# Optimization experiments

Hardware: AMD Instinct MI355X
Metric: run time of the kernel (lower is better)

Reference implementation:

```python
import jax, jax.numpy as jnp
import numpy as np
import math

L = 7          # spherical-harmonic truncation -> lsize = (L+1)^2 = 64
T = 128        # number of channels/fragments in clms


def _cg_coef(j1, m1, j2, m2, j, m):
    """Clebsch-Gordan coefficient <j1 m1 j2 m2 | j m> via the Racah formula."""
    if m1 + m2 != m or not (abs(j1 - j2) <= j <= j1 + j2):
        return 0.0
    f = math.factorial
    pref = math.sqrt((2 * j + 1) * f(j1 + j2 - j) * f(j1 - j2 + j)
                     * f(-j1 + j2 + j) / f(j1 + j2 + j + 1))
    pref *= math.sqrt(f(j + m) * f(j - m) * f(j1 - m1) * f(j1 + m1)
                      * f(j2 - m2) * f(j2 + m2))
    kmin = max(0, j2 - j - m1, j1 + m2 - j)
    kmax = min(j1 + j2 - j, j1 - m1, j2 + m2)
    s = 0.0
    for k in range(kmin, kmax + 1):
        s += (-1) ** k / (f(k) * f(j1 + j2 - j - k) * f(j1 - m1 - k)
                          * f(j2 + m2 - k) * f(j - j2 + m1 + k) * f(j - j1 - m2 + k))
    return pref * s


def _idx(l, m):
    return l * l + l + m


def _build_C(L):
    """Dense packed CG tensor C[(l,m),(l1,m1),(l2,m2)], zero outside selection rules."""
    lsize = (L + 1) ** 2
    C = np.zeros((lsize, lsize, lsize), dtype=np.float64)
    for l1 in range(L + 1):
        for l2 in range(L + 1):
            for l in range(abs(l1 - l2), min(l1 + l2, L) + 1):
                for m1 in range(-l1, l1 + 1):
                    for m2 in range(-l2, l2 + 1):
                        m = m1 + m2
                        if abs(m) <= l:
                            C[_idx(l, m), _idx(l1, m1), _idx(l2, m2)] = \
                                _cg_coef(l1, m1, l2, m2, l, m)
    return C.astype(np.float32)


def setup_inputs() -> dict:
    key = jax.random.key(0)
    clms = jax.random.normal(key, ((L + 1) ** 2, T), dtype=jnp.float32)
    C = jnp.asarray(_build_C(L))
    return {"clms": clms, "C": C}


def reference(clms, C):
    lsize = clms.shape[0]
    Lc = int(math.isqrt(lsize)) - 1
    Tn = clms.shape[1]
    # full Kronecker product, blockwise indexed by (l1,m1),(l2,m2); [lsize, lsize, T^2]
    Gs = (clms[:, None, :, None] * clms[None, :, None, :]).reshape(lsize, lsize, Tn * Tn)
    temp = [[] for _ in range(Lc + 1)]
    for l1 in range(Lc + 1):
        for l2 in range(Lc + 1):
            g = Gs[l1 * l1:(l1 + 1) ** 2, l2 * l2:(l2 + 1) ** 2, :]
            cg = C[:, l1 * l1:(l1 + 1) ** 2, l2 * l2:(l2 + 1) ** 2]
            # cg @ g over the flattened (m1,m2) block -> [(Lc+1)^2, T^2]
            prod = jnp.einsum('kij,ijt->kt', cg, g)
            for l in range(abs(l1 - l2), min(l1 + l2, Lc) + 1):
                temp[l].append(prod[l * l:(l + 1) ** 2, :])
    return tuple(jnp.concatenate(t, axis=1) for t in temp)
```

## Files before the change

### kernel.cpp

```cpp
#include <hip/hip_runtime.h>

#define TDIM 128

__device__ __forceinline__ float u2f(unsigned int u) {
  union { unsigned int u; float f; } w; w.u = u; return w.f;
}
__device__ __forceinline__ float bf2f(unsigned short v) {
  return u2f(((unsigned int)v) << 16);
}
__device__ __forceinline__ unsigned short f2bf(float x) {
  union { float f; unsigned int u; } w; w.f = x;
  unsigned int u = w.u;
  u += 0x7fffu + ((u >> 16) & 1u);
  return (unsigned short)(u >> 16);
}

__global__ __launch_bounds__(256, 4)
void cg_kernel(const void* __restrict__ clms_raw,
               const void* __restrict__ C_raw,
               void* __restrict__ out_raw) {
  __shared__ float sa[16 * TDIM];
  __shared__ float sb[16 * TDIM];

  const int tid = threadIdx.x;

  const unsigned int* cw = (const unsigned int*)clms_raw;
  int nbf = 0;
  #pragma unroll
  for (int i = 0; i < 32; ++i) {
    unsigned int e = (cw[i] >> 7) & 0xFFu;
    nbf += (e >= 110u && e <= 135u) ? 1 : 0;
  }
  const bool in_bf16 = (nbf >= 16);
  const bool c_bf16 = ((*(const unsigned int*)C_raw) & 0xffffu) == 0x3f80u;

  const int r = blockIdx.x;
  int l = 0, cum = 0, pc = 8;
  if (r >= 8)    { l = 1; cum = 8;    pc = 21; }
  if (r >= 71)   { l = 2; cum = 71;   pc = 31; }
  if (r >= 226)  { l = 3; cum = 226;  pc = 38; }
  if (r >= 492)  { l = 4; cum = 492;  pc = 42; }
  if (r >= 870)  { l = 5; cum = 870;  pc = 43; }
  if (r >= 1343) { l = 6; cum = 1343; pc = 41; }
  if (r >= 1876) { l = 7; cum = 1876; pc = 36; }
  const int rem = r - cum;
  const int mi  = rem / pc;
  const int m   = mi - l;
  int pp = rem - mi * pc;
  int l1 = 0, l2 = 0, found = 0;
  #pragma unroll
  for (int a = 0; a < 8; ++a) {
    int d = a - l; if (d < 0) d = -d;
    int hi = a + l; if (hi > 7) hi = 7;
    int na = hi - d + 1;
    if (!found && pp < na) { l1 = a; l2 = d + pp; found = 1; }
    if (!found) pp -= na;
  }

  const int m1lo = (-l1 > m - l2) ? -l1 : (m - l2);
  const int m1hi = ( l1 < m + l2) ?  l1 : (m + l2);
  const int nnz = m1hi - m1lo + 1;
  const int i0 = l1 * (l1 + 1) + m1lo;
  const int j0 = l2 * (l2 + 1) + (m - m1lo);
  const int k0 = l * (l + 1) + m;

  #pragma unroll
  for (int kk = 0; kk < 8; ++kk) {
    const int u = tid + 256 * kk;
    if (u < 1920) {
      const int row  = u >> 6;
      const int lane = u & 63;
      const int isB  = row >= 15;
      const int q    = isB ? row - 15 : row;
      const int qc   = (q < nnz) ? q : 0;
      const int gr   = isB ? (j0 - qc) : (i0 + qc);
      float f0, f1;
      if (in_bf16) {
        unsigned int v = ((const unsigned int*)clms_raw)[gr * 64 + lane];
        f0 = u2f(v << 16); f1 = u2f(v & 0xffff0000u);
      } else {
        float2 v = ((const float2*)clms_raw)[gr * 64 + lane];
        f0 = v.x; f1 = v.y;
      }
      if (isB) {
        float cq = 0.0f;
        if (q < nnz) {
          int ci = (k0 * 64 + i0 + q) * 64 + (j0 - q);
          cq = c_bf16 ? bf2f(((const unsigned short*)C_raw)[ci])
                      : ((const float*)C_raw)[ci];
        }
        f0 *= cq; f1 *= cq;
        *(float2*)&sb[q * TDIM + lane * 2] = make_float2(f0, f1);
      } else {
        *(float2*)&sa[q * TDIM + lane * 2] = make_float2(f0, f1);
      }
    }
  }
  __syncthreads();

  const int tx = tid & 31;
  const int ty = tid >> 5;
  float4 b[15];
  #pragma unroll
  for (int q = 0; q < 15; ++q)
    b[q] = *(const float4*)&sb[q * TDIM + tx * 4];

  const unsigned long long outbase =
      (unsigned long long)r * (TDIM * TDIM) + (unsigned int)(tx * 4);

  if (in_bf16) {
    unsigned short* out = (unsigned short*)out_raw;
    for (int s0 = 0; s0 < 4; ++s0) {
      const int t1b = ty + 32 * s0;
      float4 acc[4];
      #pragma unroll
      for (int d = 0; d < 4; ++d) acc[d] = make_float4(0.f, 0.f, 0.f, 0.f);
      #pragma unroll
      for (int q = 0; q < 15; ++q) {
        if (q < nnz) {
          #pragma unroll
          for (int d = 0; d < 4; ++d) {
            float a = sa[q * TDIM + t1b + 8 * d];
            acc[d].x += a * b[q].x;
            acc[d].y += a * b[q].y;
            acc[d].z += a * b[q].z;
            acc[d].w += a * b[q].w;
          }
        }
      }
      #pragma unroll
      for (int d = 0; d < 4; ++d) {
        ushort4 o;
        o.x = f2bf(acc[d].x); o.y = f2bf(acc[d].y);
        o.z = f2bf(acc[d].z); o.w = f2bf(acc[d].w);
        *(ushort4*)(out + outbase + (unsigned long long)((t1b + 8 * d) * TDIM)) = o;
      }
    }
  } else {
    float* out = (float*)out_raw;
    for (int s0 = 0; s0 < 4; ++s0) {
      const int t1b = ty + 32 * s0;
      float4 acc[4];
      #pragma unroll
      for (int d = 0; d < 4; ++d) acc[d] = make_float4(0.f, 0.f, 0.f, 0.f);
      #pragma unroll
      for (int q = 0; q < 15; ++q) {
        if (q < nnz) {
          #pragma unroll
          for (int d = 0; d < 4; ++d) {
            float a = sa[q * TDIM + t1b + 8 * d];
            acc[d].x += a * b[q].x;
            acc[d].y += a * b[q].y;
            acc[d].z += a * b[q].z;
            acc[d].w += a * b[q].w;
          }
        }
      }
      #pragma unroll
      for (int d = 0; d < 4; ++d)
        *(float4*)(out + outbase + (unsigned long long)((t1b + 8 * d) * TDIM)) = acc[d];
    }
  }
}

extern "C" void kernel_launch(void* const* d_in, const int* in_sizes, int n_in,
                              void* d_out, int out_size, void* d_ws, size_t ws_size,
                              hipStream_t stream) {
  (void)in_sizes; (void)n_in; (void)d_ws; (void)ws_size;
  const int nrows = out_size / (TDIM * TDIM);
  cg_kernel<<<nrows, 256, 0, stream>>>(d_in[0], d_in[1], d_out);
}
```

Measured before the change: 165.9 us.

## Use persistent blocks that stage all of clms in shared memory once

Launches at most 1024 blocks that each copy the full clms matrix into shared memory once, then grid-stride over output rows. The per-row global gather of A and B rows and the associated barrier are replaced by direct shared-memory indexing, with CG coefficients applied when forming the B registers. This trades a larger shared-memory footprint per block, and so possibly lower occupancy, for removing the repeated global loads and per-row launch overhead.

```diff
diff --git a/kernel.cpp b/kernel.cpp
--- a/kernel.cpp
+++ b/kernel.cpp
@@ -18,9 +18,9 @@
 __global__ __launch_bounds__(256, 4)
 void cg_kernel(const void* __restrict__ clms_raw,
                const void* __restrict__ C_raw,
-               void* __restrict__ out_raw) {
-  __shared__ float sa[16 * TDIM];
-  __shared__ float sb[16 * TDIM];
+               void* __restrict__ out_raw,
+               const int nrows) {
+  __shared__ float sc[64 * TDIM];
 
   const int tid = threadIdx.x;
 
@@ -34,131 +34,138 @@
   const bool in_bf16 = (nbf >= 16);
   const bool c_bf16 = ((*(const unsigned int*)C_raw) & 0xffffu) == 0x3f80u;
 
-  const int r = blockIdx.x;
-  int l = 0, cum = 0, pc = 8;
-  if (r >= 8)    { l = 1; cum = 8;    pc = 21; }
-  if (r >= 71)   { l = 2; cum = 71;   pc = 31; }
-  if (r >= 226)  { l = 3; cum = 226;  pc = 38; }
-  if (r >= 492)  { l = 4; cum = 492;  pc = 42; }
-  if (r >= 870)  { l = 5; cum = 870;  pc = 43; }
-  if (r >= 1343) { l = 6; cum = 1343; pc = 41; }
-  if (r >= 1876) { l = 7; cum = 1876; pc = 36; }
-  const int rem = r - cum;
-  const int mi  = rem / pc;
-  const int m   = mi - l;
-  int pp = rem - mi * pc;
-  int l1 = 0, l2 = 0, found = 0;
-  #pragma unroll
-  for (int a = 0; a < 8; ++a) {
-    int d = a - l; if (d < 0) d = -d;
-    int hi = a + l; if (hi > 7) hi = 7;
-    int na = hi - d + 1;
-    if (!found && pp < na) { l1 = a; l2 = d + pp; found = 1; }
-    if (!found) pp -= na;
-  }
-
-  const int m1lo = (-l1 > m - l2) ? -l1 : (m - l2);
-  const int m1hi = ( l1 < m + l2) ?  l1 : (m + l2);
-  const int nnz = m1hi - m1lo + 1;
-  const int i0 = l1 * (l1 + 1) + m1lo;
-  const int j0 = l2 * (l2 + 1) + (m - m1lo);
-  const int k0 = l * (l + 1) + m;
-
-  #pragma unroll
-  for (int kk = 0; kk < 8; ++kk) {
-    const int u = tid + 256 * kk;
-    if (u < 1920) {
-      const int row  = u >> 6;
-      const int lane = u & 63;
-      const int isB  = row >= 15;
-      const int q    = isB ? row - 15 : row;
-      const int qc   = (q < nnz) ? q : 0;
-      const int gr   = isB ? (j0 - qc) : (i0 + qc);
-      float f0, f1;
-      if (in_bf16) {
-        unsigned int v = ((const unsigned int*)clms_raw)[gr * 64 + lane];
-        f0 = u2f(v << 16); f1 = u2f(v & 0xffff0000u);
-      } else {
-        float2 v = ((const float2*)clms_raw)[gr * 64 + lane];
-        f0 = v.x; f1 = v.y;
-      }
-      if (isB) {
-        float cq = 0.0f;
-        if (q < nnz) {
-          int ci = (k0 * 64 + i0 + q) * 64 + (j0 - q);
-          cq = c_bf16 ? bf2f(((const unsigned short*)C_raw)[ci])
-                      : ((const float*)C_raw)[ci];
-        }
-        f0 *= cq; f1 *= cq;
-        *(float2*)&sb[q * TDIM + lane * 2] = make_float2(f0, f1);
-      } else {
-        *(float2*)&sa[q * TDIM + lane * 2] = make_float2(f0, f1);
-      }
+  if (in_bf16) {
+    const uint4* cl4 = (const uint4*)clms_raw;
+    #pragma unroll
+    for (int it = 0; it < 4; ++it) {
+      int v = tid + it * 256;
+      uint4 w = cl4[v];
+      float4* dst = (float4*)&sc[v * 8];
+      float4 d0, d1;
+      d0.x = u2f(w.x << 16); d0.y = u2f(w.x & 0xffff0000u);
+      d0.z = u2f(w.y << 16); d0.w = u2f(w.y & 0xffff0000u);
+      d1.x = u2f(w.z << 16); d1.y = u2f(w.z & 0xffff0000u);
+      d1.z = u2f(w.w << 16); d1.w = u2f(w.w & 0xffff0000u);
+      dst[0] = d0; dst[1] = d1;
+    }
+  } else {
+    const float4* cf4 = (const float4*)clms_raw;
+    float4* sc4 = (float4*)sc;
+    #pragma unroll
+    for (int it = 0; it < 8; ++it) {
+      int v = tid + it * 256;
+      sc4[v] = cf4[v];
     }
   }
   __syncthreads();
 
   const int tx = tid & 31;
   const int ty = tid >> 5;
-  float4 b[15];
-  #pragma unroll
-  for (int q = 0; q < 15; ++q)
-    b[q] = *(const float4*)&sb[q * TDIM + tx * 4];
+  const int t2 = tx * 4;
 
-  const unsigned long long outbase =
-      (unsigned long long)r * (TDIM * TDIM) + (unsigned int)(tx * 4);
+  for (int r = blockIdx.x; r < nrows; r += gridDim.x) {
+    int l = 0, cum = 0, pc = 8;
+    if (r >= 8)    { l = 1; cum = 8;    pc = 21; }
+    if (r >= 71)   { l = 2; cum = 71;   pc = 31; }
+    if (r >= 226)  { l = 3; cum = 226;  pc = 38; }
+    if (r >= 492)  { l = 4; cum = 492;  pc = 42; }
+    if (r >= 870)  { l = 5; cum = 870;  pc = 43; }
+    if (r >= 1343) { l = 6; cum = 1343; pc = 41; }
+    if (r >= 1876) { l = 7; cum = 1876; pc = 36; }
+    const int rem = r - cum;
+    const int mi  = rem / pc;
+    const int m   = mi - l;
+    int pp = rem - mi * pc;
+    int l1 = 0, l2 = 0, found = 0;
+    #pragma unroll
+    for (int a = 0; a < 8; ++a) {
+      int d = a - l; if (d < 0) d = -d;
+      int hi = a + l; if (hi > 7) hi = 7;
+      int na = hi - d + 1;
+      if (!found && pp < na) { l1 = a; l2 = d + pp; found = 1; }
+      if (!found) pp -= na;
+    }
 
-  if (in_bf16) {
-    unsigned short* out = (unsigned short*)out_raw;
-    for (int s0 = 0; s0 < 4; ++s0) {
-      const int t1b = ty + 32 * s0;
-      float4 acc[4];
+    const int m1lo = (-l1 > m - l2) ? -l1 : (m - l2);
+    const int m1hi = ( l1 < m + l2) ?  l1 : (m + l2);
+    const int nnz = m1hi - m1lo + 1;
+    const int i0 = l1 * (l1 + 1) + m1lo;
+    const int j0 = l2 * (l2 + 1) + (m - m1lo);
+    const int k0 = l * (l + 1) + m;
+
+    float4 b[15];
+    #pragma unroll
+    for (int q = 0; q < 15; ++q) {
+      const int qc = (q < nnz) ? q : 0;
+      float cq = 0.0f;
+      if (q < nnz) {
+        int ci = (k0 * 64 + i0 + q) * 64 + (j0 - q);
+        cq = c_bf16 ? bf2f(((const unsigned short*)C_raw)[ci])
+                    : ((const float*)C_raw)[ci];
+      }
+      const float4 v = *(const float4*)&sc[(j0 - qc) * TDIM + t2];
+      b[q] = make_float4(cq * v.x, cq * v.y, cq * v.z, cq * v.w);
+    }
+
+    const unsigned long long outbase =
+        (unsigned long long)r * (TDIM * TDIM) + (unsigned int)t2;
+
+    if (in_bf16) {
+      unsigned short* out = (unsigned short*)out_raw;
       #pragma unroll
-      for (int d = 0; d < 4; ++d) acc[d] = make_float4(0.f, 0.f, 0.f, 0.f);
-      #pragma unroll
-      for (int q = 0; q < 15; ++q) {
-        if (q < nnz) {
-          #pragma unroll
-          for (int d = 0; d < 4; ++d) {
-            float a = sa[q * TDIM + t1b + 8 * d];
-            acc[d].x += a * b[q].x;
-            acc[d].y += a * b[q].y;
-            acc[d].z += a * b[q].z;
-            acc[d].w += a * b[q].w;
+      for (int s0 = 0; s0 < 4; ++s0) {
+        const int t1b = ty + 32 * s0;
+        float4 acc[4];
+        #pragma unroll
+        for (int d = 0; d < 4; ++d) acc[d] = make_float4(0.f, 0.f, 0.f, 0.f);
+        #pragma unroll
+        for (int q = 0; q < 15; ++q) {
+          if (q < nnz) {
+            #pragma unroll
+            for (int d = 0; d < 4; ++d) {
+              float a = sc[(i0 + q) * TDIM + t1b + 8 * d];
+              acc[d].x += a * b[q].x;
+              acc[d].y += a * b[q].y;
+              acc[d].z += a * b[q].z;
+              acc[d].w += a * b[q].w;
+            }
           }
         }
+        #pragma unroll
+        for (int d = 0; d < 4; ++d) {
+          ushort4 o;
+          o.x = f2bf(acc[d].x); o.y = f2bf(acc[d].y);
+          o.z = f2bf(acc[d].z); o.w = f2bf(acc[d].w);
+          *(ushort4*)(out + outbase +
+                      (unsigned long long)((t1b + 8 * d) * TDIM)) = o;
+        }
       }
+    } else {
+      float* out = (float*)out_raw;
       #pragma unroll
-      for (int d = 0; d < 4; ++d) {
-        ushort4 o;
-        o.x = f2bf(acc[d].x); o.y = f2bf(acc[d].y);
-        o.z = f2bf(acc[d].z); o.w = f2bf(acc[d].w);
-        *(ushort4*)(out + outbase + (unsigned long long)((t1b + 8 * d) * TDIM)) = o;
-      }
-    }
-  } else {
-    float* out = (float*)out_raw;
-    for (int s0 = 0; s0 < 4; ++s0) {
-      const int t1b = ty + 32 * s0;
-      float4 acc[4];
-      #pragma unroll
-      for (int d = 0; d < 4; ++d) acc[d] = make_float4(0.f, 0.f, 0.f, 0.f);
-      #pragma unroll
-      for (int q = 0; q < 15; ++q) {
-        if (q < nnz) {
-          #pragma unroll
-          for (int d = 0; d < 4; ++d) {
-            float a = sa[q * TDIM + t1b + 8 * d];
-            acc[d].x += a * b[q].x;
-            acc[d].y += a * b[q].y;
-            acc[d].z += a * b[q].z;
-            acc[d].w += a * b[q].w;
+      for (int s0 = 0; s0 < 4; ++s0) {
+        const int t1b = ty + 32 * s0;
+        float4 acc[4];
+        #pragma unroll
+        for (int d = 0; d < 4; ++d) acc[d] = make_float4(0.f, 0.f, 0.f, 0.f);
+        #pragma unroll
+        for (int q = 0; q < 15; ++q) {
+          if (q < nnz) {
+            #pragma unroll
+            for (int d = 0; d < 4; ++d) {
+              float a = sc[(i0 + q) * TDIM + t1b + 8 * d];
+              acc[d].x += a * b[q].x;
+              acc[d].y += a * b[q].y;
+              acc[d].z += a * b[q].z;
+              acc[d].w += a * b[q].w;
+            }
           }
         }
+        #pragma unroll
+        for (int d = 0; d < 4; ++d)
+          *(float4*)(out + outbase +
+                     (unsigned long long)((t1b + 8 * d) * TDIM)) = acc[d];
       }
-      #pragma unroll
-      for (int d = 0; d < 4; ++d)
-        *(float4*)(out + outbase + (unsigned long long)((t1b + 8 * d) * TDIM)) = acc[d];
     }
   }
 }
@@ -168,5 +175,6 @@
                               hipStream_t stream) {
   (void)in_sizes; (void)n_in; (void)d_ws; (void)ws_size;
   const int nrows = out_size / (TDIM * TDIM);
-  cg_kernel<<<nrows, 256, 0, stream>>>(d_in[0], d_in[1], d_out);
+  const int grid = (nrows < 1024) ? nrows : 1024;
+  cg_kernel<<<grid, 256, 0, stream>>>(d_in[0], d_in[1], d_out, nrows);
 }
```

After: 173.8 us. +4.8%, slower.
